# Kernel tuning notes

Measured on AMD Instinct MI355X. Metric: run time of the kernel, lower is better.

The kernel has to match this reference:

```python
import jax, jax.numpy as jnp
import numpy as np

N_HEADS = 8
EPS = 1e-6


def setup_inputs() -> dict:
    key = jax.random.key(0)
    ks = jax.random.split(key, 9)
    B, L, E = 4, 4096, 512
    s = 1.0 / np.sqrt(E)
    return {
        "x": jax.random.normal(ks[0], (B, L, E), jnp.float32),
        "Wq": jax.random.normal(ks[1], (E, E), jnp.float32) * s,
        "bq": jax.random.normal(ks[2], (E,), jnp.float32) * 0.01,
        "Wk": jax.random.normal(ks[3], (E, E), jnp.float32) * s,
        "bk": jax.random.normal(ks[4], (E,), jnp.float32) * 0.01,
        "Wv": jax.random.normal(ks[5], (E, E), jnp.float32) * s,
        "bv": jax.random.normal(ks[6], (E,), jnp.float32) * 0.01,
        "Wo": jax.random.normal(ks[7], (E, E), jnp.float32) * s,
        "bo": jax.random.normal(ks[8], (E,), jnp.float32) * 0.01,
    }


def reference(x, Wq, bq, Wk, bk, Wv, bv, Wo, bo):
    # x: (B, L, E); self-attention so query = key = value = x
    B, L, E = x.shape
    H = N_HEADS
    d = E // H
    m = jnp.float32(L)  # m = max(src_len, tgt_len)

    # projections (torch Linear: x @ W.T + b), then ReLU feature map
    q = jax.nn.relu(x @ Wq.T + bq).reshape(B, L, H, d)
    k = jax.nn.relu(x @ Wk.T + bk).reshape(B, L, H, d)
    v = (x @ Wv.T + bv).reshape(B, L, H, d)

    # cosFormer positional reweighting: (pi/2) * i / m for i = 1..L
    idx = (jnp.pi / 2.0) * jnp.arange(1, L + 1, dtype=jnp.float32) / m  # (L,)
    sin = jnp.sin(idx)[None, :, None, None]  # (1, L, 1, 1)
    cos = jnp.cos(idx)[None, :, None, None]

    q_sin, q_cos = q * sin, q * cos
    k_sin, k_cos = k * sin, k * cos

    # non-causal linear attention: per-head kv state, O(L * d^2)
    kv_cos = jnp.einsum("blhk,blhd->bhkd", k_cos, v)  # (B, H, d, d)
    kv_sin = jnp.einsum("blhk,blhd->bhkd", k_sin, v)

    k_cos_sum = k_cos.sum(axis=1)  # (B, H, d)
    k_sin_sum = k_sin.sum(axis=1)

    z = 1.0 / jnp.maximum(
        jnp.einsum("blhd,bhd->blh", q_cos, k_cos_sum)
        + jnp.einsum("blhd,bhd->blh", q_sin, k_sin_sum),
        EPS,
    )  # (B, L, H)

    attn = (
        jnp.einsum("blhk,bhkd->blhd", q_cos, kv_cos)
        + jnp.einsum("blhk,bhkd->blhd", q_sin, kv_sin)
    ) * z[..., None]

    out = attn.reshape(B, L, E) @ Wo.T + bo  # (B, L, E)
    return out
```

## Files before the change

### kernel.cpp

```cpp
#include <hip/hip_runtime.h>
#include <hip/hip_bf16.h>

#define L_SEQ 4096
#define E_DIM 512
#define NHEAD 8
#define DHEAD 64
#define NBATCH 4
#define NROWS (NBATCH * L_SEQ)

typedef short bf16x8 __attribute__((ext_vector_type(8)));
typedef float f32x4 __attribute__((ext_vector_type(4)));

__device__ __forceinline__ float bf2f(ushort u) {
    union { float f; unsigned int i; } x;
    x.i = ((unsigned int)u) << 16;
    return x.f;
}
__device__ __forceinline__ ushort f2bf(float f) {
    unsigned int u = __float_as_uint(f);
    unsigned int r = 0x7fffu + ((u >> 16) & 1u);
    u += r;
    return (ushort)(u >> 16);
}

#define GLD16(gptr, lptr) \
    __builtin_amdgcn_global_load_lds( \
        (const __attribute__((address_space(1))) void*)(gptr), \
        (__attribute__((address_space(3))) void*)(lptr), 16, 0, 0)

#define BAR_LGKM() do { \
    asm volatile("s_waitcnt lgkmcnt(0)" ::: "memory"); \
    __builtin_amdgcn_sched_barrier(0); \
    __builtin_amdgcn_s_barrier(); \
    __builtin_amdgcn_sched_barrier(0); } while (0)

__global__ void convert_kernel(const float* __restrict__ in, ushort* __restrict__ out, int n4) {
    int stride = gridDim.x * blockDim.x;
    for (int i = blockIdx.x * blockDim.x + threadIdx.x; i < n4; i += stride) {
        float4 f = reinterpret_cast<const float4*>(in)[i];
        ushort4 o;
        o.x = f2bf(f.x); o.y = f2bf(f.y); o.z = f2bf(f.z); o.w = f2bf(f.w);
        reinterpret_cast<ushort4*>(out)[i] = o;
    }
}

__global__ __launch_bounds__(256) void convert_w_kernel(
    const float* __restrict__ w0, const float* __restrict__ w1,
    const float* __restrict__ w2, const float* __restrict__ w3,
    ushort* __restrict__ o0, ushort* __restrict__ o1,
    ushort* __restrict__ o2, ushort* __restrict__ o3,
    float* __restrict__ sintab, float* __restrict__ costab)
{
    const int tid = threadIdx.x;
    const int y = blockIdx.y;
    if (y == 4) {
        const int l = blockIdx.x * 256 + tid;
        if (blockIdx.x < 16) {
            const float ang = (float)(l + 1) * (1.5707963267948966f / (float)L_SEQ);
            sintab[l] = sinf(ang);
            costab[l] = cosf(ang);
        }
        return;
    }
    const float* in = (y == 0) ? w0 : (y == 1) ? w1 : (y == 2) ? w2 : w3;
    ushort* out = (y == 0) ? o0 : (y == 1) ? o1 : (y == 2) ? o2 : o3;
    const int i = blockIdx.x * 256 + tid;
    float4 f = reinterpret_cast<const float4*>(in)[i];
    ushort4 o;
    o.x = f2bf(f.x); o.y = f2bf(f.y); o.z = f2bf(f.z); o.w = f2bf(f.w);
    reinterpret_cast<ushort4*>(out)[i] = o;
}

template<int MODE_BASE>
__global__ __launch_bounds__(256, 2) void gemm6_kernel(
    const ushort* __restrict__ A,
    const ushort* __restrict__ wq, const ushort* __restrict__ wk,
    const ushort* __restrict__ wv, const ushort* __restrict__ wo,
    const float* __restrict__ bq, const float* __restrict__ bk,
    const float* __restrict__ bv, const float* __restrict__ bo,
    ushort* __restrict__ qb, ushort* __restrict__ kT, ushort* __restrict__ vT,
    float* __restrict__ outF)
{
    __shared__ ushort SH[32768];
    ushort* TS = SH;

    const int tid = threadIdx.x;
    const int lane = tid & 63;
    const int wid = tid >> 6;
    const int wm = wid >> 1;
    const int wn = wid & 1;
    const int rowBase = blockIdx.x * 128;

    int mode, colBase;
    if (MODE_BASE == 3) { mode = 3; colBase = blockIdx.y * 128; }
    else { mode = blockIdx.y >> 2; colBase = (blockIdx.y & 3) * 128; }

    const ushort* __restrict__ W =
        (mode == 0) ? wq : (mode == 1) ? wk : (mode == 2) ? wv : wo;
    const float* __restrict__ bias =
        (mode == 0) ? bq : (mode == 1) ? bk : (mode == 2) ? bv : bo;

    const int fr = lane & 15;
    const int g = lane >> 4;
    const int fr7 = fr & 7;
    const int sc_row = tid >> 3;
    const int sc_c16 = tid & 7;

    f32x4 acc[4][4];
#pragma unroll
    for (int m = 0; m < 4; ++m)
#pragma unroll
        for (int n = 0; n < 4; ++n)
            acc[m][n] = (f32x4){0.f, 0.f, 0.f, 0.f};

    auto STAGE = [&](int kt) {
        const int k0 = kt * 64;
        const int bufb = (kt & 1) * 16384;
#pragma unroll
        for (int i = 0; i < 4; ++i) {
            const int row = i * 32 + sc_row;
            const int srcc = (sc_c16 ^ (row & 7)) * 8;
            GLD16(&A[(size_t)(rowBase + row) * E_DIM + k0 + srcc],
                  &SH[bufb + row * 64 + sc_c16 * 8]);
        }
#pragma unroll
        for (int i = 0; i < 4; ++i) {
            const int row = i * 32 + sc_row;
            const int srcc = (sc_c16 ^ (row & 7)) * 8;
            GLD16(&W[(size_t)(colBase + row) * E_DIM + k0 + srcc],
                  &SH[bufb + 8192 + row * 64 + sc_c16 * 8]);
        }
    };

    STAGE(0);
    STAGE(1);
    asm volatile("s_waitcnt vmcnt(8)" ::: "memory");
    __builtin_amdgcn_sched_barrier(0);
    __builtin_amdgcn_s_barrier();
    __builtin_amdgcn_sched_barrier(0);

    const int kch0 = (g ^ fr7) * 8;
    const int kch1 = ((4 + g) ^ fr7) * 8;
    const int aroff = (wm * 64 + fr) * 64;
    const int broff = 8192 + (wn * 64 + fr) * 64;
    const int b = rowBase >> 12;
    const int lloc = rowBase & (L_SEQ - 1);

    for (int gt = 0; gt < 8; ++gt) {
        const int base = (gt & 1) * 16384;
        bf16x8 af[2][4], bfv[2][4];
#pragma unroll
        for (int m = 0; m < 4; ++m) {
            af[0][m] = *reinterpret_cast<const bf16x8*>(&SH[base + aroff + m * 1024 + kch0]);
            af[1][m] = *reinterpret_cast<const bf16x8*>(&SH[base + aroff + m * 1024 + kch1]);
        }
#pragma unroll
        for (int n = 0; n < 4; ++n) {
            bfv[0][n] = *reinterpret_cast<const bf16x8*>(&SH[base + broff + n * 1024 + kch0]);
            bfv[1][n] = *reinterpret_cast<const bf16x8*>(&SH[base + broff + n * 1024 + kch1]);
        }
        BAR_LGKM();

        if (gt + 2 < 8) STAGE(gt + 2);

        __builtin_amdgcn_s_setprio(1);
#pragma unroll
        for (int kk = 0; kk < 2; ++kk)
#pragma unroll
            for (int m = 0; m < 4; ++m)
#pragma unroll
                for (int n = 0; n < 4; ++n)
                    acc[m][n] = __builtin_amdgcn_mfma_f32_16x16x32_bf16(
                        af[kk][m], bfv[kk][n], acc[m][n], 0, 0, 0);
        __builtin_amdgcn_s_setprio(0);
        __builtin_amdgcn_sched_barrier(0);

        if (gt < 7) {
            if (gt + 2 < 8) asm volatile("s_waitcnt vmcnt(8)" ::: "memory");
            else            asm volatile("s_waitcnt vmcnt(0)" ::: "memory");
            __builtin_amdgcn_sched_barrier(0);
            __builtin_amdgcn_s_barrier();
            __builtin_amdgcn_sched_barrier(0);
        }
    }

    if (mode == 0) {
#pragma unroll
        for (int m = 0; m < 4; ++m)
#pragma unroll
            for (int j = 0; j < 4; ++j) {
                const int grow = rowBase + wm * 64 + m * 16 + g * 4 + j;
#pragma unroll
                for (int n = 0; n < 4; ++n) {
                    const int gcol = colBase + wn * 64 + n * 16 + fr;
                    const float val = fmaxf(acc[m][n][j] + bias[gcol], 0.f);
                    qb[(size_t)grow * E_DIM + gcol] = f2bf(val);
                }
            }
    } else if (mode == 3) {
#pragma unroll
        for (int m = 0; m < 4; ++m)
#pragma unroll
            for (int j = 0; j < 4; ++j) {
                const int grow = rowBase + wm * 64 + m * 16 + g * 4 + j;
#pragma unroll
                for (int n = 0; n < 4; ++n) {
                    const int gcol = colBase + wn * 64 + n * 16 + fr;
                    outF[(size_t)grow * E_DIM + gcol] = acc[m][n][j] + bias[gcol];
                }
            }
    } else {
        ushort* __restrict__ dstbuf = (mode == 1) ? kT : vT;
        __syncthreads();
#pragma unroll
        for (int m = 0; m < 4; ++m)
#pragma unroll
            for (int j = 0; j < 4; ++j) {
                const int lr_ = wm * 64 + m * 16 + g * 4 + j;
#pragma unroll
                for (int n = 0; n < 4; ++n) {
                    const int fcl = wn * 64 + n * 16 + fr;
                    float val = acc[m][n][j] + bias[colBase + fcl];
                    if (mode == 1) val = fmaxf(val, 0.f);
                    TS[fcl * 136 + lr_] = f2bf(val);
                }
            }
        __syncthreads();
#pragma unroll
        for (int i = 0; i < 8; ++i) {
            const int c = i * 256 + tid;
            const int r = c >> 4;
            const int cc = c & 15;
            const size_t dst = ((size_t)(b * E_DIM + colBase + r)) * L_SEQ + lloc + cc * 8;
            *reinterpret_cast<uint4*>(&dstbuf[dst]) =
                *reinterpret_cast<const uint4*>(&TS[r * 136 + cc * 8]);
        }
    }
}

__global__ __launch_bounds__(256) void kv_kernel(
    const ushort* __restrict__ kT, const ushort* __restrict__ vT,
    const float* __restrict__ sintab, const float* __restrict__ costab,
    float* __restrict__ kv_part, float* __restrict__ sum_part)
{
    const int chunk = blockIdx.x;
    const int bh = blockIdx.y;
    const int tid = threadIdx.x;
    const int lane = tid & 63;
    const int w = tid >> 6;
    const int fr = lane & 15;
    const int g = lane >> 4;

    const size_t tbase = (size_t)bh * 64 * L_SEQ;

    f32x4 acc[8], accS[8];
#pragma unroll
    for (int n = 0; n < 8; ++n) {
        acc[n] = (f32x4){0.f, 0.f, 0.f, 0.f};
        accS[n] = (f32x4){0.f, 0.f, 0.f, 0.f};
    }

    const int lchunk = chunk * (L_SEQ / 8);
    for (int l0 = lchunk; l0 < lchunk + (L_SEQ / 8); l0 += 32) {
        const int col = l0 + g * 8;
        bf16x8 vf = *reinterpret_cast<const bf16x8*>(&vT[tbase + (size_t)(w * 16 + fr) * L_SEQ + col]);
        bf16x8 kf[4];
#pragma unroll
        for (int n = 0; n < 4; ++n)
            kf[n] = *reinterpret_cast<const bf16x8*>(&kT[tbase + (size_t)(n * 16 + fr) * L_SEQ + col]);
        float4 c0 = *reinterpret_cast<const float4*>(&costab[col]);
        float4 c1 = *reinterpret_cast<const float4*>(&costab[col + 4]);
        float4 s0 = *reinterpret_cast<const float4*>(&sintab[col]);
        float4 s1 = *reinterpret_cast<const float4*>(&sintab[col + 4]);
        const float c8[8] = {c0.x, c0.y, c0.z, c0.w, c1.x, c1.y, c1.z, c1.w};
        const float s8[8] = {s0.x, s0.y, s0.z, s0.w, s1.x, s1.y, s1.z, s1.w};
        bf16x8 afc, afs, cw, sw;
#pragma unroll
        for (int e = 0; e < 8; ++e) {
            const float v = bf2f((ushort)vf[e]);
            afc[e] = (short)f2bf(v * c8[e]);
            afs[e] = (short)f2bf(v * s8[e]);
            cw[e]  = (short)f2bf(c8[e]);
            sw[e]  = (short)f2bf(s8[e]);
        }
#pragma unroll
        for (int n = 0; n < 4; ++n) {
            acc[n]      = __builtin_amdgcn_mfma_f32_16x16x32_bf16(afc, kf[n], acc[n], 0, 0, 0);
            acc[n + 4]  = __builtin_amdgcn_mfma_f32_16x16x32_bf16(afs, kf[n], acc[n + 4], 0, 0, 0);
            accS[n]     = __builtin_amdgcn_mfma_f32_16x16x32_bf16(cw,  kf[n], accS[n], 0, 0, 0);
            accS[n + 4] = __builtin_amdgcn_mfma_f32_16x16x32_bf16(sw,  kf[n], accS[n + 4], 0, 0, 0);
        }
    }

    const size_t pbase = ((size_t)(chunk * 32 + bh)) * 8192;
#pragma unroll
    for (int n = 0; n < 8; ++n)
#pragma unroll
        for (int j = 0; j < 4; ++j)
            kv_part[pbase + (size_t)(w * 16 + g * 4 + j) * 128 + n * 16 + fr] = acc[n][j];
    if (w == 0 && g == 0) {
        const size_t sbase = (size_t)(chunk * 32 + bh) * 128;
#pragma unroll
        for (int n = 0; n < 8; ++n)
            sum_part[sbase + n * 16 + fr] = accS[n][0];
    }
}

#define KVT_ROWS 80
#define KVT_STRIDE (KVT_ROWS * 128)
__global__ __launch_bounds__(256) void kv_reduce_kernel(
    const float* __restrict__ kv_part, const float* __restrict__ sum_part,
    ushort* __restrict__ kvT)
{
    const int bh = blockIdx.x;
    const int tid = threadIdx.x;
    ushort* kvb = kvT + (size_t)bh * KVT_STRIDE;
    for (int idx = tid; idx < 8192; idx += 256) {
        float s = 0.f;
#pragma unroll
        for (int c = 0; c < 8; ++c)
            s += kv_part[((size_t)(c * 32 + bh)) * 8192 + idx];
        kvb[idx] = f2bf(s);
    }
    if (tid < 128) {
        float s = 0.f;
#pragma unroll
        for (int c = 0; c < 8; ++c)
            s += sum_part[(size_t)(c * 32 + bh) * 128 + tid];
        const ushort hi = f2bf(s);
        const float lo = s - bf2f(hi);
        kvb[64 * 128 + tid] = hi;
        kvb[65 * 128 + tid] = f2bf(lo);
    }
    for (int idx = tid; idx < 14 * 128; idx += 256)
        kvb[66 * 128 + idx] = 0;
}

__global__ __launch_bounds__(256) void attn_kernel(
    const ushort* __restrict__ Qb, const ushort* __restrict__ kvT,
    const float* __restrict__ sintab, const float* __restrict__ costab,
    ushort* __restrict__ attn_out)
{
    const int bh = blockIdx.y;
    const int b = bh >> 3, h = bh & 7;
    const int tid = threadIdx.x;
    const int lane = tid & 63;
    const int w = tid >> 6;

    __shared__ ushort Bs[KVT_ROWS][136];

#pragma unroll
    for (int i = 0; i < 5; ++i) {
        const int c = i * 256 + tid;
        const int d = c >> 4, cc = c & 15;
        *reinterpret_cast<uint4*>(&Bs[d][cc * 8]) =
            *reinterpret_cast<const uint4*>(&kvT[(size_t)bh * KVT_STRIDE + (size_t)c * 8]);
    }
    __syncthreads();

    const int rowBase = blockIdx.x * 256 + w * 64;
    const int fr = lane & 15;
    const int g = lane >> 4;

    float cvm[4], svm[4];
#pragma unroll
    for (int m = 0; m < 4; ++m) {
        const int l = (rowBase + m * 16 + fr) & (L_SEQ - 1);
        cvm[m] = costab[l];
        svm[m] = sintab[l];
    }

    f32x4 acc[4][5];
#pragma unroll
    for (int m = 0; m < 4; ++m)
#pragma unroll
        for (int n = 0; n < 5; ++n)
            acc[m][n] = (f32x4){0.f, 0.f, 0.f, 0.f};

#pragma unroll
    for (int ks = 0; ks < 4; ++ks) {
        const int kk = (ks & 1) * 32 + g * 8;
        const int kcomb = ks * 32 + g * 8;

        bf16x8 af[4];
#pragma unroll
        for (int m = 0; m < 4; ++m) {
            const int r = rowBase + m * 16 + fr;
            bf16x8 qf = *reinterpret_cast<const bf16x8*>(
                &Qb[((size_t)(b * L_SEQ) + r) * E_DIM + h * DHEAD + kk]);
            const float sc = (ks < 2) ? cvm[m] : svm[m];
#pragma unroll
            for (int e = 0; e < 8; ++e)
                af[m][e] = (short)f2bf(bf2f((ushort)qf[e]) * sc);
        }

        bf16x8 bfr[5];
#pragma unroll
        for (int n = 0; n < 5; ++n)
            bfr[n] = *reinterpret_cast<const bf16x8*>(&Bs[n * 16 + fr][kcomb]);
#pragma unroll
        for (int m = 0; m < 4; ++m)
#pragma unroll
            for (int n = 0; n < 5; ++n)
                acc[m][n] = __builtin_amdgcn_mfma_f32_16x16x32_bf16(af[m], bfr[n], acc[m][n], 0, 0, 0);
    }

#pragma unroll
    for (int m = 0; m < 4; ++m) {
#pragma unroll
        for (int j = 0; j < 4; ++j) {
            const float den = __shfl(acc[m][4][j], g * 16 + 0) + __shfl(acc[m][4][j], g * 16 + 1);
            const float z = 1.f / fmaxf(den, 1e-6f);
            const int grow = rowBase + m * 16 + g * 4 + j;
            const size_t obase = ((size_t)(b * L_SEQ) + grow) * E_DIM + h * DHEAD;
#pragma unroll
            for (int n = 0; n < 4; ++n)
                attn_out[obase + n * 16 + fr] = f2bf(acc[m][n][j] * z);
        }
    }
}

extern "C" void kernel_launch(void* const* d_in, const int* in_sizes, int n_in,
                              void* d_out, int out_size, void* d_ws, size_t ws_size,
                              hipStream_t stream) {
    const float* x  = (const float*)d_in[0];
    const float* Wq = (const float*)d_in[1];
    const float* bq = (const float*)d_in[2];
    const float* Wk = (const float*)d_in[3];
    const float* bk = (const float*)d_in[4];
    const float* Wv = (const float*)d_in[5];
    const float* bv = (const float*)d_in[6];
    const float* Wo = (const float*)d_in[7];
    const float* bo = (const float*)d_in[8];
    float* out = (float*)d_out;

    char* ws = (char*)d_ws;
    size_t off = 0;
    auto alloc = [&](size_t bytes) -> char* {
        char* p = ws + off;
        off += (bytes + 255) & ~(size_t)255;
        return p;
    };

    const size_t big = (size_t)NROWS * E_DIM * sizeof(ushort);
    ushort* xb  = (ushort*)alloc(big);
    ushort* wqb = (ushort*)alloc(512 * 512 * sizeof(ushort));
    ushort* wkb = (ushort*)alloc(512 * 512 * sizeof(ushort));
    ushort* wvb = (ushort*)alloc(512 * 512 * sizeof(ushort));
    ushort* wob = (ushort*)alloc(512 * 512 * sizeof(ushort));
    ushort* qb  = (ushort*)alloc(big);
    ushort* kT  = (ushort*)alloc(big);
    ushort* vT  = (ushort*)alloc(big);
    float* kv_part  = (float*)alloc((size_t)8 * 32 * 8192 * sizeof(float));
    float* sum_part = (float*)alloc((size_t)8 * 32 * 128 * sizeof(float));
    ushort* kvT     = (ushort*)alloc((size_t)32 * KVT_STRIDE * sizeof(ushort));
    float* sintab   = (float*)alloc(L_SEQ * sizeof(float));
    float* costab   = (float*)alloc(L_SEQ * sizeof(float));
    ushort* attnb = kT;

    convert_kernel<<<2048, 256, 0, stream>>>(x, xb, NROWS * E_DIM / 4);
    convert_w_kernel<<<dim3(256, 5), 256, 0, stream>>>(
        Wq, Wk, Wv, Wo, wqb, wkb, wvb, wob, sintab, costab);

    gemm6_kernel<0><<<dim3(128, 12), 256, 0, stream>>>(
        xb, wqb, wkb, wvb, wob, bq, bk, bv, bo, qb, kT, vT, nullptr);

    kv_kernel<<<dim3(8, 32), 256, 0, stream>>>(kT, vT, sintab, costab, kv_part, sum_part);
    kv_reduce_kernel<<<32, 256, 0, stream>>>(kv_part, sum_part, kvT);

    attn_kernel<<<dim3(16, 32), 256, 0, stream>>>(qb, kvT, sintab, costab, attnb);

    gemm6_kernel<3><<<dim3(128, 4), 256, 0, stream>>>(
        attnb, wqb, wkb, wvb, wob, bq, bk, bv, bo, nullptr, nullptr, nullptr, out);
}
```

Before: 97.40 us.

## Fuse fp32-to-bf16 conversion of x into the QKV projection GEMM

```diff
diff --git a/kernel.cpp b/kernel.cpp
--- a/kernel.cpp
+++ b/kernel.cpp
@@ -33,16 +33,6 @@
     __builtin_amdgcn_sched_barrier(0); \
     __builtin_amdgcn_s_barrier(); \
     __builtin_amdgcn_sched_barrier(0); } while (0)
-
-__global__ void convert_kernel(const float* __restrict__ in, ushort* __restrict__ out, int n4) {
-    int stride = gridDim.x * blockDim.x;
-    for (int i = blockIdx.x * blockDim.x + threadIdx.x; i < n4; i += stride) {
-        float4 f = reinterpret_cast<const float4*>(in)[i];
-        ushort4 o;
-        o.x = f2bf(f.x); o.y = f2bf(f.y); o.z = f2bf(f.z); o.w = f2bf(f.w);
-        reinterpret_cast<ushort4*>(out)[i] = o;
-    }
-}
 
 __global__ __launch_bounds__(256) void convert_w_kernel(
     const float* __restrict__ w0, const float* __restrict__ w1,
@@ -71,17 +61,13 @@
     reinterpret_cast<ushort4*>(out)[i] = o;
 }
 
-template<int MODE_BASE>
-__global__ __launch_bounds__(256, 2) void gemm6_kernel(
-    const ushort* __restrict__ A,
-    const ushort* __restrict__ wq, const ushort* __restrict__ wk,
-    const ushort* __restrict__ wv, const ushort* __restrict__ wo,
-    const float* __restrict__ bq, const float* __restrict__ bk,
-    const float* __restrict__ bv, const float* __restrict__ bo,
-    ushort* __restrict__ qb, ushort* __restrict__ kT, ushort* __restrict__ vT,
-    float* __restrict__ outF)
+__global__ __launch_bounds__(256, 3) void qkv8_kernel(
+    const float* __restrict__ X,
+    const ushort* __restrict__ wq, const ushort* __restrict__ wk, const ushort* __restrict__ wv,
+    const float* __restrict__ bq, const float* __restrict__ bk, const float* __restrict__ bv,
+    ushort* __restrict__ qb, ushort* __restrict__ kT, ushort* __restrict__ vT)
 {
-    __shared__ ushort SH[32768];
+    __shared__ ushort SH[24576];
     ushort* TS = SH;
 
     const int tid = threadIdx.x;
@@ -90,21 +76,14 @@
     const int wm = wid >> 1;
     const int wn = wid & 1;
     const int rowBase = blockIdx.x * 128;
-
-    int mode, colBase;
-    if (MODE_BASE == 3) { mode = 3; colBase = blockIdx.y * 128; }
-    else { mode = blockIdx.y >> 2; colBase = (blockIdx.y & 3) * 128; }
-
-    const ushort* __restrict__ W =
-        (mode == 0) ? wq : (mode == 1) ? wk : (mode == 2) ? wv : wo;
-    const float* __restrict__ bias =
-        (mode == 0) ? bq : (mode == 1) ? bk : (mode == 2) ? bv : bo;
+    const int mode = blockIdx.y >> 2;
+    const int colBase = (blockIdx.y & 3) * 128;
+
+    const ushort* __restrict__ W = (mode == 0) ? wq : (mode == 1) ? wk : wv;
+    const float* __restrict__ bias = (mode == 0) ? bq : (mode == 1) ? bk : bv;
 
     const int fr = lane & 15;
     const int g = lane >> 4;
-    const int fr7 = fr & 7;
-    const int sc_row = tid >> 3;
-    const int sc_c16 = tid & 7;
 
     f32x4 acc[4][4];
 #pragma unroll
@@ -114,70 +93,88 @@
             acc[m][n] = (f32x4){0.f, 0.f, 0.f, 0.f};
 
     auto STAGE = [&](int kt) {
-        const int k0 = kt * 64;
-        const int bufb = (kt & 1) * 16384;
+        const int k0 = kt * 32;
+        char* bufc = (char*)SH + (kt & 1) * 24576;
 #pragma unroll
         for (int i = 0; i < 4; ++i) {
-            const int row = i * 32 + sc_row;
-            const int srcc = (sc_c16 ^ (row & 7)) * 8;
-            GLD16(&A[(size_t)(rowBase + row) * E_DIM + k0 + srcc],
-                  &SH[bufb + row * 64 + sc_c16 * 8]);
-        }
-#pragma unroll
-        for (int i = 0; i < 4; ++i) {
-            const int row = i * 32 + sc_row;
-            const int srcc = (sc_c16 ^ (row & 7)) * 8;
-            GLD16(&W[(size_t)(colBase + row) * E_DIM + k0 + srcc],
-                  &SH[bufb + 8192 + row * 64 + sc_c16 * 8]);
+            const int c = i * 256 + tid;
+            const int row = c >> 3;
+            const int slot = c & 7;
+            const int src = (slot ^ (row & 7)) * 4;
+            GLD16(&X[(size_t)(rowBase + row) * E_DIM + k0 + src],
+                  bufc + (row * 32 + slot * 4) * 4);
+        }
+#pragma unroll
+        for (int i = 0; i < 2; ++i) {
+            const int c = i * 256 + tid;
+            const int row = c >> 2;
+            const int slot = c & 3;
+            const int src = (slot ^ ((row >> 1) & 3)) * 8;
+            GLD16(&W[(size_t)(colBase + row) * E_DIM + k0 + src],
+                  bufc + 16384 + (row * 32 + slot * 8) * 2);
         }
     };
 
     STAGE(0);
     STAGE(1);
-    asm volatile("s_waitcnt vmcnt(8)" ::: "memory");
+    asm volatile("s_waitcnt vmcnt(6)" ::: "memory");
     __builtin_amdgcn_sched_barrier(0);
     __builtin_amdgcn_s_barrier();
     __builtin_amdgcn_sched_barrier(0);
 
-    const int kch0 = (g ^ fr7) * 8;
-    const int kch1 = ((4 + g) ^ fr7) * 8;
-    const int aroff = (wm * 64 + fr) * 64;
-    const int broff = 8192 + (wn * 64 + fr) * 64;
     const int b = rowBase >> 12;
     const int lloc = rowBase & (L_SEQ - 1);
 
-    for (int gt = 0; gt < 8; ++gt) {
-        const int base = (gt & 1) * 16384;
-        bf16x8 af[2][4], bfv[2][4];
+    for (int gt = 0; gt < 16; ++gt) {
+        const char* bufc = (const char*)SH + (gt & 1) * 24576;
+        const float* Af = (const float*)bufc;
+        const ushort* Bf = (const ushort*)(bufc + 16384);
+
+        f32x4 alo[4], ahi[4];
+        bf16x8 bfv[4];
 #pragma unroll
         for (int m = 0; m < 4; ++m) {
-            af[0][m] = *reinterpret_cast<const bf16x8*>(&SH[base + aroff + m * 1024 + kch0]);
-            af[1][m] = *reinterpret_cast<const bf16x8*>(&SH[base + aroff + m * 1024 + kch1]);
+            const int r = wm * 64 + m * 16 + fr;
+            const int s0 = (2 * g) ^ (r & 7);
+            const int s1 = (2 * g + 1) ^ (r & 7);
+            alo[m] = *reinterpret_cast<const f32x4*>(&Af[r * 32 + s0 * 4]);
+            ahi[m] = *reinterpret_cast<const f32x4*>(&Af[r * 32 + s1 * 4]);
         }
 #pragma unroll
         for (int n = 0; n < 4; ++n) {
-            bfv[0][n] = *reinterpret_cast<const bf16x8*>(&SH[base + broff + n * 1024 + kch0]);
-            bfv[1][n] = *reinterpret_cast<const bf16x8*>(&SH[base + broff + n * 1024 + kch1]);
+            const int r = wn * 64 + n * 16 + fr;
+            const int sl = g ^ ((r >> 1) & 3);
+            bfv[n] = *reinterpret_cast<const bf16x8*>(&Bf[r * 32 + sl * 8]);
         }
         BAR_LGKM();
 
-        if (gt + 2 < 8) STAGE(gt + 2);
+        if (gt + 2 < 16) STAGE(gt + 2);
+
+        bf16x8 af[4];
+#pragma unroll
+        for (int m = 0; m < 4; ++m) {
+            const int hilo = g & 1;
+#pragma unroll
+            for (int e = 0; e < 4; ++e) {
+                af[m][e]     = (short)f2bf(alo[m][e]);
+                af[m][e + 4] = (short)f2bf(ahi[m][e]);
+            }
+            (void)hilo;
+        }
 
         __builtin_amdgcn_s_setprio(1);
 #pragma unroll
-        for (int kk = 0; kk < 2; ++kk)
-#pragma unroll
-            for (int m = 0; m < 4; ++m)
-#pragma unroll
-                for (int n = 0; n < 4; ++n)
-                    acc[m][n] = __builtin_amdgcn_mfma_f32_16x16x32_bf16(
-                        af[kk][m], bfv[kk][n], acc[m][n], 0, 0, 0);
+        for (int m = 0; m < 4; ++m)
+#pragma unroll
+            for (int n = 0; n < 4; ++n)
+                acc[m][n] = __builtin_amdgcn_mfma_f32_16x16x32_bf16(
+                    af[m], bfv[n], acc[m][n], 0, 0, 0);
         __builtin_amdgcn_s_setprio(0);
         __builtin_amdgcn_sched_barrier(0);
 
-        if (gt < 7) {
-            if (gt + 2 < 8) asm volatile("s_waitcnt vmcnt(8)" ::: "memory");
-            else            asm volatile("s_waitcnt vmcnt(0)" ::: "memory");
+        if (gt < 15) {
+            if (gt + 2 < 16) asm volatile("s_waitcnt vmcnt(6)" ::: "memory");
+            else             asm volatile("s_waitcnt vmcnt(0)" ::: "memory");
             __builtin_amdgcn_sched_barrier(0);
             __builtin_amdgcn_s_barrier();
             __builtin_amdgcn_sched_barrier(0);
@@ -195,18 +192,6 @@
                     const int gcol = colBase + wn * 64 + n * 16 + fr;
                     const float val = fmaxf(acc[m][n][j] + bias[gcol], 0.f);
                     qb[(size_t)grow * E_DIM + gcol] = f2bf(val);
-                }
-            }
-    } else if (mode == 3) {
-#pragma unroll
-        for (int m = 0; m < 4; ++m)
-#pragma unroll
-            for (int j = 0; j < 4; ++j) {
-                const int grow = rowBase + wm * 64 + m * 16 + g * 4 + j;
-#pragma unroll
-                for (int n = 0; n < 4; ++n) {
-                    const int gcol = colBase + wn * 64 + n * 16 + fr;
-                    outF[(size_t)grow * E_DIM + gcol] = acc[m][n][j] + bias[gcol];
                 }
             }
     } else {
@@ -236,6 +221,115 @@
                 *reinterpret_cast<const uint4*>(&TS[r * 136 + cc * 8]);
         }
     }
+}
+
+__global__ __launch_bounds__(256, 2) void out_gemm_kernel(
+    const ushort* __restrict__ A, const ushort* __restrict__ W,
+    const float* __restrict__ bias, float* __restrict__ outF)
+{
+    __shared__ ushort SH[32768];
+
+    const int tid = threadIdx.x;
+    const int lane = tid & 63;
+    const int wid = tid >> 6;
+    const int wm = wid >> 1;
+    const int wn = wid & 1;
+    const int rowBase = blockIdx.x * 128;
+    const int colBase = blockIdx.y * 128;
+
+    const int fr = lane & 15;
+    const int g = lane >> 4;
+    const int fr7 = fr & 7;
+    const int sc_row = tid >> 3;
+    const int sc_c16 = tid & 7;
+
+    f32x4 acc[4][4];
+#pragma unroll
+    for (int m = 0; m < 4; ++m)
+#pragma unroll
+        for (int n = 0; n < 4; ++n)
+            acc[m][n] = (f32x4){0.f, 0.f, 0.f, 0.f};
+
+    auto STAGE = [&](int kt) {
+        const int k0 = kt * 64;
+        const int bufb = (kt & 1) * 16384;
+#pragma unroll
+        for (int i = 0; i < 4; ++i) {
+            const int row = i * 32 + sc_row;
+            const int srcc = (sc_c16 ^ (row & 7)) * 8;
+            GLD16(&A[(size_t)(rowBase + row) * E_DIM + k0 + srcc],
+                  &SH[bufb + row * 64 + sc_c16 * 8]);
+        }
+#pragma unroll
+        for (int i = 0; i < 4; ++i) {
+            const int row = i * 32 + sc_row;
+            const int srcc = (sc_c16 ^ (row & 7)) * 8;
+            GLD16(&W[(size_t)(colBase + row) * E_DIM + k0 + srcc],
+                  &SH[bufb + 8192 + row * 64 + sc_c16 * 8]);
+        }
+    };
+
+    STAGE(0);
+    STAGE(1);
+    asm volatile("s_waitcnt vmcnt(8)" ::: "memory");
+    __builtin_amdgcn_sched_barrier(0);
+    __builtin_amdgcn_s_barrier();
+    __builtin_amdgcn_sched_barrier(0);
+
+    const int kch0 = (g ^ fr7) * 8;
+    const int kch1 = ((4 + g) ^ fr7) * 8;
+    const int aroff = (wm * 64 + fr) * 64;
+    const int broff = 8192 + (wn * 64 + fr) * 64;
+
+    for (int gt = 0; gt < 8; ++gt) {
+        const int base = (gt & 1) * 16384;
+        bf16x8 af[2][4], bfv[2][4];
+#pragma unroll
+        for (int m = 0; m < 4; ++m) {
+            af[0][m] = *reinterpret_cast<const bf16x8*>(&SH[base + aroff + m * 1024 + kch0]);
+            af[1][m] = *reinterpret_cast<const bf16x8*>(&SH[base + aroff + m * 1024 + kch1]);
+        }
+#pragma unroll
+        for (int n = 0; n < 4; ++n) {
+            bfv[0][n] = *reinterpret_cast<const bf16x8*>(&SH[base + broff + n * 1024 + kch0]);
+            bfv[1][n] = *reinterpret_cast<const bf16x8*>(&SH[base + broff + n * 1024 + kch1]);
+        }
+        BAR_LGKM();
+
+        if (gt + 2 < 8) STAGE(gt + 2);
+
+        __builtin_amdgcn_s_setprio(1);
+#pragma unroll
+        for (int kk = 0; kk < 2; ++kk)
+#pragma unroll
+            for (int m = 0; m < 4; ++m)
+#pragma unroll
+                for (int n = 0; n < 4; ++n)
+                    acc[m][n] = __builtin_amdgcn_mfma_f32_16x16x32_bf16(
+                        af[kk][m], bfv[kk][n], acc[m][n], 0, 0, 0);
+        __builtin_amdgcn_s_setprio(0);
+        __builtin_amdgcn_sched_barrier(0);
+
+        if (gt < 7) {
+            if (gt + 2 < 8) asm volatile("s_waitcnt vmcnt(8)" ::: "memory");
+            else            asm volatile("s_waitcnt vmcnt(0)" ::: "memory");
+            __builtin_amdgcn_sched_barrier(0);
+            __builtin_amdgcn_s_barrier();
+            __builtin_amdgcn_sched_barrier(0);
+        }
+    }
+
+#pragma unroll
+    for (int m = 0; m < 4; ++m)
+#pragma unroll
+        for (int j = 0; j < 4; ++j) {
+            const int grow = rowBase + wm * 64 + m * 16 + g * 4 + j;
+#pragma unroll
+            for (int n = 0; n < 4; ++n) {
+                const int gcol = colBase + wn * 64 + n * 16 + fr;
+                outF[(size_t)grow * E_DIM + gcol] = acc[m][n][j] + bias[gcol];
+            }
+        }
 }
 
 __global__ __launch_bounds__(256) void kv_kernel(
@@ -443,7 +537,6 @@
     };
 
     const size_t big = (size_t)NROWS * E_DIM * sizeof(ushort);
-    ushort* xb  = (ushort*)alloc(big);
     ushort* wqb = (ushort*)alloc(512 * 512 * sizeof(ushort));
     ushort* wkb = (ushort*)alloc(512 * 512 * sizeof(ushort));
     ushort* wvb = (ushort*)alloc(512 * 512 * sizeof(ushort));
@@ -458,18 +551,16 @@
     float* costab   = (float*)alloc(L_SEQ * sizeof(float));
     ushort* attnb = kT;
 
-    convert_kernel<<<2048, 256, 0, stream>>>(x, xb, NROWS * E_DIM / 4);
     convert_w_kernel<<<dim3(256, 5), 256, 0, stream>>>(
         Wq, Wk, Wv, Wo, wqb, wkb, wvb, wob, sintab, costab);
 
-    gemm6_kernel<0><<<dim3(128, 12), 256, 0, stream>>>(
-        xb, wqb, wkb, wvb, wob, bq, bk, bv, bo, qb, kT, vT, nullptr);
+    qkv8_kernel<<<dim3(128, 12), 256, 0, stream>>>(
+        x, wqb, wkb, wvb, bq, bk, bv, qb, kT, vT);
 
     kv_kernel<<<dim3(8, 32), 256, 0, stream>>>(kT, vT, sintab, costab, kv_part, sum_part);
     kv_reduce_kernel<<<32, 256, 0, stream>>>(kv_part, sum_part, kvT);
 
     attn_kernel<<<dim3(16, 32), 256, 0, stream>>>(qb, kvT, sintab, costab, attnb);
 
-    gemm6_kernel<3><<<dim3(128, 4), 256, 0, stream>>>(
-        attnb, wqb, wkb, wvb, wob, bq, bk, bv, bo, nullptr, nullptr, nullptr, out);
-}
+    out_gemm_kernel<<<dim3(128, 4), 256, 0, stream>>>(attnb, wob, bo, out);
+}
```

After: 106.1 us. 1.09x slower.
